# Kernel tuning notes

Hardware: AMD Instinct MI355X
Metric: run time of the kernel (lower is better)

Reference implementation:

```python
import jax, jax.numpy as jnp
import numpy as np

K = 5  # spline kernel size per dim (dim=3 -> 125 kernels)
N1, E1 = 10000, 60000
N2, E2 = 2500, 15000
N3, E3 = 625, 3750
N4, E4 = 160, 960
NC = 4  # num part classes (ShapeNet 'Pistol')


def spline_conv(x, ei, u, W, R, b):
    """SplineConv with degree-1 open B-splines, dim=3, kernel_size=K.
    x: [N, in], ei: [2, E] (src, dst), u: [E, 3] pseudo coords in [0,1],
    W: [K^3, in, out], R: [in, out] root weight, b: [out] bias.
    Mean-normalized neighborhood aggregation (norm=True) + root + bias."""
    src, dst = ei[0], ei[1]
    N, E = x.shape[0], ei.shape[1]
    v = u * (K - 1)
    k0f = jnp.clip(jnp.floor(v), 0.0, K - 2)
    f = v - k0f  # fractional offsets in [0, 1]
    k0 = k0f.astype(jnp.int32)
    # Pre-transform node features by every kernel: z[n, k, o]
    z = jnp.einsum('ni,kio->nko', x, W)
    msg = jnp.zeros((E, W.shape[2]), x.dtype)
    for b0 in (0, 1):
        for b1 in (0, 1):
            for b2 in (0, 1):
                idx = (k0[:, 0] + b0) * K * K + (k0[:, 1] + b1) * K + (k0[:, 2] + b2)
                wgt = ((f[:, 0] if b0 else 1.0 - f[:, 0]) *
                       (f[:, 1] if b1 else 1.0 - f[:, 1]) *
                       (f[:, 2] if b2 else 1.0 - f[:, 2]))
                msg = msg + wgt[:, None] * z[src, idx]
    agg = jax.ops.segment_sum(msg, dst, num_segments=N)
    deg = jax.ops.segment_sum(jnp.ones((E,), x.dtype), dst, num_segments=N)
    return agg / jnp.maximum(deg, 1.0)[:, None] + x @ R + b


def _net(x, u1, u2, u3, u4, w1, r1, b1, w12, r12, b12, w2, r2, b2, w22, r22, b22,
         w3, r3, b3, w32, r32, b32, w4, r4, b4, w42, r42, b42, w5, r5, b5,
         w6, r6, b6, w7, r7, b7, fc1w, fc1b, fc2w, fc2b,
         sk1w, sk1b, sk2w, sk2b, sk3w, sk3b, ei1, ei2, ei3, ei4, c1, c2, c3):
    elu = jax.nn.elu
    h1 = elu(spline_conv(x, ei1, u1, w1, r1, b1))
    h1 = elu(spline_conv(h1, ei1, u1, w12, r12, b12))
    h2 = jnp.concatenate([jax.ops.segment_max(h1, c1, num_segments=N2),
                          jnp.ones((N2, 1), x.dtype)], axis=1)
    h2 = elu(spline_conv(h2, ei2, u2, w2, r2, b2))
    h2 = elu(spline_conv(h2, ei2, u2, w22, r22, b22))
    h3 = jnp.concatenate([jax.ops.segment_max(h2, c2, num_segments=N3),
                          jnp.ones((N3, 1), x.dtype)], axis=1)
    h3 = elu(spline_conv(h3, ei3, u3, w3, r3, b3))
    h3 = elu(spline_conv(h3, ei3, u3, w32, r32, b32))
    h4 = jnp.concatenate([jax.ops.segment_max(h3, c3, num_segments=N4),
                          jnp.ones((N4, 1), x.dtype)], axis=1)
    h4 = elu(spline_conv(h4, ei4, u4, w4, r4, b4))
    h4 = elu(spline_conv(h4, ei4, u4, w42, r42, b42))
    h4 = elu(spline_conv(h4, ei4, u4, w42, r42, b42))  # conv42 applied twice, as in source
    h4 = elu(h4 @ fc1w + fc1b)  # dropout omitted (eval mode)
    g3 = elu(spline_conv(h4[c3] + h3 @ sk3w + sk3b, ei3, u3, w5, r5, b5))
    g2 = elu(spline_conv(g3[c2] + h2 @ sk2w + sk2b, ei2, u2, w6, r6, b6))
    g1 = elu(spline_conv(g2[c1] + h1 @ sk1w + sk1b, ei1, u1, w7, r7, b7))
    return jax.nn.log_softmax(g1 @ fc2w + fc2b, axis=1)


def setup_inputs() -> dict:
    key = jax.random.key(0)
    ks = iter(jax.random.split(key, 96))

    def nrm(shape, s=0.1):
        return jax.random.normal(next(ks), shape, jnp.float32) * s

    def edges(E, N):
        return jax.random.randint(next(ks), (2, E), 0, N, dtype=jnp.int32)

    def clus(Nl, Nn):
        # surjective cluster assignment so every pooled voxel is non-empty
        extra = jax.random.randint(next(ks), (Nl - Nn,), 0, Nn, dtype=jnp.int32)
        return jnp.concatenate([jnp.arange(Nn, dtype=jnp.int32), extra])

    d = {}
    d['x'] = nrm((N1, 1), 1.0)
    d['ei1'], d['u1'] = edges(E1, N1), jax.random.uniform(next(ks), (E1, 3), jnp.float32)
    d['ei2'], d['u2'] = edges(E2, N2), jax.random.uniform(next(ks), (E2, 3), jnp.float32)
    d['ei3'], d['u3'] = edges(E3, N3), jax.random.uniform(next(ks), (E3, 3), jnp.float32)
    d['ei4'], d['u4'] = edges(E4, N4), jax.random.uniform(next(ks), (E4, 3), jnp.float32)
    d['c1'], d['c2'], d['c3'] = clus(N1, N2), clus(N2, N3), clus(N3, N4)
    KK = K ** 3
    for name, cin, cout in [('1', 1, 64), ('12', 64, 64), ('2', 65, 64), ('22', 64, 64),
                            ('3', 65, 64), ('32', 64, 64), ('4', 65, 64), ('42', 64, 64),
                            ('5', 32, 32), ('6', 32, 32), ('7', 32, 32)]:
        d['w' + name] = nrm((KK, cin, cout))
        d['r' + name] = nrm((cin, cout))
        d['b' + name] = jnp.zeros((cout,), jnp.float32)
    d['fc1w'], d['fc1b'] = nrm((64, 32)), jnp.zeros((32,), jnp.float32)
    d['fc2w'], d['fc2b'] = nrm((32, NC)), jnp.zeros((NC,), jnp.float32)
    for s in ('1', '2', '3'):
        d['sk' + s + 'w'] = nrm((64, 32))
        d['sk' + s + 'b'] = jnp.zeros((32,), jnp.float32)
    return d


def reference(x, u1, u2, u3, u4, w1, r1, b1, w12, r12, b12, w2, r2, b2, w22, r22, b22,
              w3, r3, b3, w32, r32, b32, w4, r4, b4, w42, r42, b42, w5, r5, b5,
              w6, r6, b6, w7, r7, b7, fc1w, fc1b, fc2w, fc2b,
              sk1w, sk1b, sk2w, sk2b, sk3w, sk3b, ei1, ei2, ei3, ei4, c1, c2, c3):
    return _net(x, u1, u2, u3, u4, w1, r1, b1, w12, r12, b12, w2, r2, b2, w22, r22, b22,
                w3, r3, b3, w32, r32, b32, w4, r4, b4, w42, r42, b42, w5, r5, b5,
                w6, r6, b6, w7, r7, b7, fc1w, fc1b, fc2w, fc2b,
                sk1w, sk1b, sk2w, sk2b, sk3w, sk3b, ei1, ei2, ei3, ei4, c1, c2, c3)
```

## Files before the change

kernel.cpp:

```cpp
#include <hip/hip_runtime.h>
#include <math.h>


static const int N1 = 10000, E1 = 60000;
static const int N2 = 2500,  E2 = 15000;
static const int N3 = 625,   E3 = 3750;
static const int N4 = 160,   E4 = 960;
static const int NC = 4;
static const int CHUNK = 64;

typedef __attribute__((ext_vector_type(8))) short bfrag;
typedef __attribute__((ext_vector_type(4))) float f32x4;

__device__ __forceinline__ float eluf(float x) { return x > 0.f ? x : expm1f(x); }

__device__ __forceinline__ unsigned short bfc(float f) {
    unsigned u = __float_as_uint(f);
    return (unsigned short)((u + 0x7FFF + ((u >> 16) & 1)) >> 16);
}

struct InitArgs {
    const float* wsrc[10]; unsigned short* wdst[10];
    int cinmat[10], xs_[10], cout[10];
    long welems[10];
    long wtot;
    float* pools[3]; int pM[3];
    float* agg; int aggN4;
    int* preblk; int preN;
    int bB, bC, bD;
};

__global__ __launch_bounds__(256) void init_misc(InitArgs A) {
    const int blk = blockIdx.x, tid = threadIdx.x;
    if (blk < A.bB) {
        const long t = (long)blk * 256 + tid;
        if (t >= A.wtot) return;
        int k = 0;
        while (t >= A.welems[k]) ++k;
        const long base = k ? A.welems[k - 1] : 0;
        const long i2 = t - base;
        const int co = A.cout[k], cm = A.cinmat[k], xs = A.xs_[k];
        const int o = (int)(i2 % co);
        const long rest = i2 / co;
        const int i = (int)(rest % cm);
        const int kk = (int)(rest / cm);
        const float v = A.wsrc[k][((size_t)kk * xs + i) * co + o];
        const int KG = cm >> 3;
        A.wdst[k][(((size_t)(kk * KG + (i >> 3))) * co + o) * 8 + (i & 7)] = bfc(v);
    } else if (blk < A.bC) {
        const int t = (blk - A.bB) * 256 + tid;
        if (t >= A.pM[2]) return;
        const int p = (t < A.pM[0]) ? 0 : (t < A.pM[1] ? 1 : 2);
        const int base = p ? A.pM[p - 1] : 0;
        const int i2 = t - base;
        A.pools[p][i2] = (i2 % 65 == 64) ? 1.0f : -INFINITY;
    } else if (blk < A.bD) {
        const int t = (blk - A.bC) * 256 + tid;
        if (t < A.aggN4) ((float4*)A.agg)[t] = make_float4(0.f, 0.f, 0.f, 0.f);
    } else {
        const int t = (blk - A.bD) * 256 + tid;
        if (t < A.preN) A.preblk[t] = 0;
    }
}

struct Levels {
    const float* u[4]; const int* ei[4]; int E[4];
    int nb0[5];
    int cb0[5];
    int mc[4];
    int* ek0[4]; int* hist[4]; int* cursor[4]; float* deg[4];
    int* bchunk0[4]; int* ck0[4]; int* ccnt[4]; int* perm[4];
};

__global__ __launch_bounds__(256) void prep_conv1(Levels L, const float* __restrict__ x,
                                                  const float* __restrict__ w1,
                                                  float* __restrict__ agg, int nbTot) {
    __shared__ int lh[64];
    const int tid = threadIdx.x;
    if ((int)blockIdx.x < nbTot) {
        int l = 0;
        while (l < 3 && (int)blockIdx.x >= L.nb0[l + 1]) ++l;
        const int bl = blockIdx.x - L.nb0[l];
        if (tid < 64) lh[tid] = 0;
        __syncthreads();
        const int e = bl * 256 + tid;
        if (e < L.E[l]) {
            int b = 0;
            #pragma unroll
            for (int d = 0; d < 3; ++d) {
                const float v = L.u[l][e * 3 + d] * 4.0f;
                const float kf = fminf(fmaxf(floorf(v), 0.f), 3.f);
                b = (b << 2) | (int)kf;
            }
            L.ek0[l][e] = b;
            atomicAdd(&lh[b], 1);
            atomicAdd(&L.deg[l][L.ei[l][L.E[l] + e]], 1.0f);
        }
        __syncthreads();
        if (tid < 64 && lh[tid]) atomicAdd(&L.hist[l][tid], lh[tid]);
    } else {
        const int t = (blockIdx.x - nbTot) * 256 + tid;
        const int e = t >> 6, o = t & 63;
        if (e >= E1) return;
        const int src = L.ei[0][e], dst = L.ei[0][E1 + e];
        float f[3]; int kb = 0;
        #pragma unroll
        for (int d = 0; d < 3; ++d) {
            const float v = L.u[0][e * 3 + d] * 4.0f;
            const float kf = fminf(fmaxf(floorf(v), 0.f), 3.f);
            f[d] = v - kf; kb = kb * 5 + (int)kf;
        }
        float s = 0.f;
        #pragma unroll
        for (int c = 0; c < 8; ++c) {
            const int b0 = (c >> 2) & 1, b1 = (c >> 1) & 1, b2 = c & 1;
            const float wgt = (b0 ? f[0] : 1.f - f[0]) * (b1 ? f[1] : 1.f - f[1]) *
                              (b2 ? f[2] : 1.f - f[2]);
            s += wgt * w1[(size_t)(kb + b0 * 25 + b1 * 5 + b2) * 64 + o];
        }
        atomicAdd(&agg[(size_t)dst * 64 + o], x[src] * s);
    }
}

__global__ void scan_all(Levels L) {
    const int l = blockIdx.x;
    __shared__ int sb[65];
    const int t = threadIdx.x;
    if (t == 0) {
        int cc = 0;
        for (int b = 0; b < 64; ++b) { sb[b] = cc; cc += (L.hist[l][b] + CHUNK - 1) / CHUNK; }
        sb[64] = cc;
    }
    __syncthreads();
    L.bchunk0[l][t] = sb[t];
    if (t == 0) L.bchunk0[l][64] = sb[64];
}

__global__ __launch_bounds__(256) void fill_scatter_node1(
        Levels L, const float* __restrict__ x, float* __restrict__ agg,
        const float* __restrict__ r1, const float* __restrict__ b1,
        float* __restrict__ h1a, int cbTot, int nbTot) {
    __shared__ int lh[64], lbase[64];
    const int tid = threadIdx.x;
    const int blk = blockIdx.x;
    if (blk < cbTot) {
        int l = 0;
        while (l < 3 && blk >= L.cb0[l + 1]) ++l;
        const int c = (blk - L.cb0[l]) * 256 + tid;
        if (c >= L.mc[l]) return;
        const int* bchunk0 = L.bchunk0[l];
        if (c >= bchunk0[64]) { L.ccnt[l][c] = 0; L.ck0[l][c] = 0; return; }
        int lo = 0, hi = 64;
        while (hi - lo > 1) { int m = (lo + hi) >> 1; if (bchunk0[m] <= c) lo = m; else hi = m; }
        const int j = c - bchunk0[lo];
        L.ck0[l][c] = lo;
        L.ccnt[l][c] = min(CHUNK, L.hist[l][lo] - j * CHUNK);
    } else if (blk < cbTot + nbTot) {
        const int fb = blk - cbTot;
        int l = 0;
        while (l < 3 && fb >= L.nb0[l + 1]) ++l;
        const int bl = fb - L.nb0[l];
        if (tid < 64) lh[tid] = 0;
        __syncthreads();
        const int e = bl * 256 + tid;
        int b = -1, r = 0;
        if (e < L.E[l]) { b = L.ek0[l][e]; r = atomicAdd(&lh[b], 1); }
        __syncthreads();
        if (tid < 64) lbase[tid] = lh[tid] ? atomicAdd(&L.cursor[l][tid], lh[tid]) : 0;
        __syncthreads();
        if (e < L.E[l]) L.perm[l][L.bchunk0[l][b] * CHUNK + lbase[b] + r] = e;
    } else {
        const int nb = blk - cbTot - nbTot;
        const int lane = tid & 63;
        const int grp  = tid >> 6;
        const int n = nb * 4 + grp;
        if (n >= N1) return;
        const float d = fmaxf(L.deg[0][n], 1.f);
        const size_t idx = (size_t)n * 64 + lane;
        float s = agg[idx] / d + b1[lane];
        agg[idx] = 0.f;
        s += x[n] * r1[lane];
        h1a[idx] = eluf(s);
    }
}

template<int CINMAT, int COUT, bool HAS_ONES>
__global__ __launch_bounds__(256) void bucket_gemm(
        const float* __restrict__ x, const int* __restrict__ ei, const float* __restrict__ u,
        const unsigned short* __restrict__ Wt, const float* __restrict__ Wf,
        const int* __restrict__ perm, const int* __restrict__ ck0, const int* __restrict__ ccnt,
        float* __restrict__ agg, int E) {
    constexpr int ALDA = CINMAT + 8;
    constexpr int KG   = CINMAT / 8;
    constexpr int NT   = COUT / 16;
    constexpr int HALVES = CINMAT / 32;
    constexpr int XS   = CINMAT + (HAS_ONES ? 1 : 0);
    constexpr int IT   = CINMAT / 4;

    __shared__ unsigned short A0s[64 * ALDA], A1s[64 * ALDA];
    __shared__ float gS[64 * 4], sS[64 * 2];
    __shared__ int srcS[64], dstS[64];
    __shared__ float WonesS[HAS_ONES ? 8 * COUT : 4];

    const int chunk = blockIdx.x;
    const int cnt = ccnt[chunk];
    if (cnt == 0) return;
    const int b = ck0[chunk];
    const int kbase = ((b >> 4) & 3) * 25 + ((b >> 2) & 3) * 5 + (b & 3);
    const int cstart = chunk * CHUNK;
    const int tid = threadIdx.x;

    if (tid < CHUNK) {
        const int e = tid;
        const int pe = (e < cnt) ? perm[cstart + e] : -1;
        int sv = -1, dv = 0;
        float g0 = 0, g1 = 0, g2 = 0, g3 = 0, s0 = 0, s1 = 0;
        if (pe >= 0) {
            sv = ei[pe]; dv = ei[E + pe];
            float f[3];
            #pragma unroll
            for (int d2 = 0; d2 < 3; ++d2) {
                const float v = u[pe * 3 + d2] * 4.f;
                const float kf = fminf(fmaxf(floorf(v), 0.f), 3.f);
                f[d2] = v - kf;
            }
            g0 = (1.f - f[0]) * (1.f - f[1]); g1 = (1.f - f[0]) * f[1];
            g2 = f[0] * (1.f - f[1]);         g3 = f[0] * f[1];
            s0 = 1.f - f[2]; s1 = f[2];
        }
        srcS[e] = sv; dstS[e] = dv;
        gS[e * 4 + 0] = g0; gS[e * 4 + 1] = g1; gS[e * 4 + 2] = g2; gS[e * 4 + 3] = g3;
        sS[e * 2 + 0] = s0; sS[e * 2 + 1] = s1;
    }
    if (HAS_ONES) {
        for (int t2 = tid; t2 < 8 * COUT; t2 += 256) {
            const int c = t2 / COUT, o = t2 % COUT;
            const int koff = ((c >> 2) & 1) * 25 + ((c >> 1) & 1) * 5 + (c & 1);
            WonesS[t2] = Wf[((size_t)(kbase + koff) * XS + CINMAT) * COUT + o];
        }
    }
    __syncthreads();

    {
        const int e  = tid >> 2;
        const int ib = (tid & 3) * IT;
        const int sv = srcS[e];
        const float sc0 = sS[e * 2], sc1 = sS[e * 2 + 1];
        #pragma unroll
        for (int j = 0; j < IT; j += 2) {
            float x0 = 0.f, x1 = 0.f;
            if (sv >= 0) {
                x0 = x[(size_t)sv * XS + ib + j];
                x1 = x[(size_t)sv * XS + ib + j + 1];
            }
            const unsigned p0 = bfc(x0 * sc0) | ((unsigned)bfc(x1 * sc0) << 16);
            const unsigned p1 = bfc(x0 * sc1) | ((unsigned)bfc(x1 * sc1) << 16);
            *(unsigned*)&A0s[e * ALDA + ib + j] = p0;
            *(unsigned*)&A1s[e * ALDA + ib + j] = p1;
        }
    }
    __syncthreads();

    const int lane = tid & 63;
    const int wid  = tid >> 6;
    const int m0   = wid * 16;
    const int arow = m0 + (lane & 15);
    const int kg   = lane >> 4;
    const int ocol = lane & 15;

    f32x4 acc[4][NT];
    #pragma unroll
    for (int q = 0; q < 4; ++q)
        #pragma unroll
        for (int nt = 0; nt < NT; ++nt) acc[q][nt] = (f32x4){0.f, 0.f, 0.f, 0.f};

    #pragma unroll
    for (int q = 0; q < 4; ++q) {
        #pragma unroll
        for (int b2 = 0; b2 < 2; ++b2) {
            const unsigned short* Ab = b2 ? A1s : A0s;
            const int koff = (q >> 1) * 25 + (q & 1) * 5 + b2;
            #pragma unroll
            for (int hf = 0; hf < HALVES; ++hf) {
                const bfrag a = *(const bfrag*)(Ab + arow * ALDA + hf * 32 + kg * 8);
                const int krow = (kbase + koff) * KG + hf * 4 + kg;
                #pragma unroll
                for (int nt = 0; nt < NT; ++nt) {
                    const bfrag bb = *(const bfrag*)(Wt + ((size_t)krow * COUT + nt * 16 + ocol) * 8);
                    acc[q][nt] = __builtin_amdgcn_mfma_f32_16x16x32_bf16(a, bb, acc[q][nt], 0, 0, 0);
                }
            }
        }
    }

    const int grp = lane >> 4;
    #pragma unroll
    for (int nt = 0; nt < NT; ++nt) {
        const int o = nt * 16 + ocol;
        float wo[8];
        if (HAS_ONES) {
            #pragma unroll
            for (int c = 0; c < 8; ++c) wo[c] = WonesS[c * COUT + o];
        }
        #pragma unroll
        for (int r = 0; r < 4; ++r) {
            const int e = m0 + grp * 4 + r;
            if (e < cnt) {
                const float g0 = gS[e * 4 + 0], g1 = gS[e * 4 + 1];
                const float g2 = gS[e * 4 + 2], g3 = gS[e * 4 + 3];
                float v = g0 * acc[0][nt][r] + g1 * acc[1][nt][r] +
                          g2 * acc[2][nt][r] + g3 * acc[3][nt][r];
                if (HAS_ONES) {
                    const float s0v = sS[e * 2], s1v = sS[e * 2 + 1];
                    v += g0 * (s0v * wo[0] + s1v * wo[1]) + g1 * (s0v * wo[2] + s1v * wo[3]) +
                         g2 * (s0v * wo[4] + s1v * wo[5]) + g3 * (s0v * wo[6] + s1v * wo[7]);
                }
                atomicAdd(&agg[(size_t)dstS[e] * COUT + o], v);
            }
        }
    }
}

enum { NODE_PLAIN = 0, NODE_SEGMAX = 1, NODE_FC1 = 2, NODE_LSM = 3 };

template<int CIN, int COUT, int MODE>
__global__ void spline_node_f(const float* __restrict__ x, float* __restrict__ agg,
                              const float* __restrict__ deg, const float* __restrict__ R,
                              const float* __restrict__ b, float* __restrict__ out, int N,
                              const int* __restrict__ cl, float* __restrict__ pool,
                              const float* __restrict__ fw, const float* __restrict__ fb2,
                              float* __restrict__ fout) {
    constexpr int NPB = 256 / COUT;
    __shared__ float rowbuf[NPB][COUT];
    const int lane = threadIdx.x % COUT;
    const int grp  = threadIdx.x / COUT;
    const int n = blockIdx.x * NPB + grp;
    if (n >= N) return;
    const float d = fmaxf(deg[n], 1.f);
    const size_t idx = (size_t)n * COUT + lane;
    float s = agg[idx] / d + b[lane];
    agg[idx] = 0.f;
    const float* xs = x + (size_t)n * CIN;
    #pragma unroll 4
    for (int i = 0; i < CIN; ++i) s += xs[i] * R[i * COUT + lane];
    const float val = eluf(s);
    if (MODE == NODE_PLAIN || MODE == NODE_SEGMAX) out[idx] = val;
    if (MODE == NODE_SEGMAX) {
        float* addr = pool + (size_t)cl[n] * 65 + lane;
        if (val >= 0.f) atomicMax((int*)addr, __float_as_int(val));
        else            atomicMin((unsigned int*)addr, __float_as_uint(val));
    }
    if (MODE == NODE_FC1) {
        rowbuf[grp][lane] = val;
        if (lane < 32) {
            float s2 = fb2[lane];
            #pragma unroll 4
            for (int i = 0; i < 64; ++i) s2 += rowbuf[grp][i] * fw[i * 32 + lane];
            fout[(size_t)n * 32 + lane] = eluf(s2);
        }
    }
    if (MODE == NODE_LSM) {
        float p[NC];
        #pragma unroll
        for (int o = 0; o < NC; ++o) p[o] = val * fw[lane * NC + o];
        #pragma unroll
        for (int m = 16; m >= 1; m >>= 1)
            #pragma unroll
            for (int o = 0; o < NC; ++o) p[o] += __shfl_xor(p[o], m, 32);
        #pragma unroll
        for (int o = 0; o < NC; ++o) p[o] += fb2[o];
        const float mx = fmaxf(fmaxf(p[0], p[1]), fmaxf(p[2], p[3]));
        float se = 0.f;
        #pragma unroll
        for (int o = 0; o < NC; ++o) se += expf(p[o] - mx);
        const float lg = logf(se);
        if (lane < NC) fout[(size_t)n * NC + lane] = p[lane] - mx - lg;
    }
}

__global__ void skip_gather(const float* __restrict__ up, const int* __restrict__ cl,
                            const float* __restrict__ h, const float* __restrict__ skw,
                            const float* __restrict__ skb, float* __restrict__ out, int N) {
    const int lane = threadIdx.x & 31;
    const int grp  = threadIdx.x >> 5;
    const int n = blockIdx.x * 8 + grp;
    if (n >= N) return;
    float s = up[(size_t)cl[n] * 32 + lane] + skb[lane];
    const float* hs = h + (size_t)n * 64;
    #pragma unroll 4
    for (int i = 0; i < 64; ++i) s += hs[i] * skw[i * 32 + lane];
    out[(size_t)n * 32 + lane] = s;
}

struct HLevel {
    const int* ei; const float* u; int E; int maxchunks;
    int *ek0, *hist, *cursor, *bchunk0, *ck0, *ccnt, *perm;
    float* deg;
};

extern "C" void kernel_launch(void* const* d_in, const int* in_sizes, int n_in,
                              void* d_out, int out_size, void* d_ws, size_t ws_size,
                              hipStream_t stream) {
    const float* x    = (const float*)d_in[0];
    const int*   ei1  = (const int*)  d_in[1];
    const float* u1   = (const float*)d_in[2];
    const int*   ei2  = (const int*)  d_in[3];
    const float* u2   = (const float*)d_in[4];
    const int*   ei3  = (const int*)  d_in[5];
    const float* u3   = (const float*)d_in[6];
    const int*   ei4  = (const int*)  d_in[7];
    const float* u4   = (const float*)d_in[8];
    const int*   c1   = (const int*)  d_in[9];
    const int*   c2   = (const int*)  d_in[10];
    const int*   c3   = (const int*)  d_in[11];
    const float *w1  = (const float*)d_in[12], *r1  = (const float*)d_in[13], *b1  = (const float*)d_in[14];
    const float *w12 = (const float*)d_in[15], *r12 = (const float*)d_in[16], *b12 = (const float*)d_in[17];
    const float *w2  = (const float*)d_in[18], *r2  = (const float*)d_in[19], *b2  = (const float*)d_in[20];
    const float *w22 = (const float*)d_in[21], *r22 = (const float*)d_in[22], *b22 = (const float*)d_in[23];
    const float *w3  = (const float*)d_in[24], *r3  = (const float*)d_in[25], *b3  = (const float*)d_in[26];
    const float *w32 = (const float*)d_in[27], *r32 = (const float*)d_in[28], *b32 = (const float*)d_in[29];
    const float *w4  = (const float*)d_in[30], *r4  = (const float*)d_in[31], *b4  = (const float*)d_in[32];
    const float *w42 = (const float*)d_in[33], *r42 = (const float*)d_in[34], *b42 = (const float*)d_in[35];
    const float *w5  = (const float*)d_in[36], *r5  = (const float*)d_in[37], *b5  = (const float*)d_in[38];
    const float *w6  = (const float*)d_in[39], *r6  = (const float*)d_in[40], *b6  = (const float*)d_in[41];
    const float *w7  = (const float*)d_in[42], *r7  = (const float*)d_in[43], *b7  = (const float*)d_in[44];
    const float *fc1w = (const float*)d_in[45], *fc1b = (const float*)d_in[46];
    const float *fc2w = (const float*)d_in[47], *fc2b = (const float*)d_in[48];
    const float *sk1w = (const float*)d_in[49], *sk1b = (const float*)d_in[50];
    const float *sk2w = (const float*)d_in[51], *sk2b = (const float*)d_in[52];
    const float *sk3w = (const float*)d_in[53], *sk3b = (const float*)d_in[54];
    float* out = (float*)d_out;

    char* wsb = (char*)d_ws;
    size_t off = 0;
    auto alloc = [&](size_t bytes) {
        void* p = wsb + off; off = (off + bytes + 255) & ~(size_t)255; return p;
    };
    auto allocF = [&](size_t n) { return (float*)alloc(n * 4); };
    auto allocI = [&](size_t n) { return (int*)alloc(n * 4); };
    auto allocH = [&](size_t n) { return (unsigned short*)alloc(n * 2); };

    float* h1a  = allocF((size_t)N1 * 64);
    float* h1   = allocF((size_t)N1 * 64);
    float* h2in = allocF((size_t)N2 * 65);
    float* h2a  = allocF((size_t)N2 * 64);
    float* h2   = allocF((size_t)N2 * 64);
    float* h3in = allocF((size_t)N3 * 65);
    float* h3a  = allocF((size_t)N3 * 64);
    float* h3   = allocF((size_t)N3 * 64);
    float* h4in = allocF((size_t)N4 * 65);
    float* h4a  = allocF((size_t)N4 * 64);
    float* h4b  = allocF((size_t)N4 * 64);
    float* h4   = allocF((size_t)N4 * 32);
    float* g3in = allocF((size_t)N3 * 32);
    float* g3   = allocF((size_t)N3 * 32);
    float* g2in = allocF((size_t)N2 * 32);
    float* g2   = allocF((size_t)N2 * 32);
    float* g1in = allocF((size_t)N1 * 32);
    float* agg  = allocF((size_t)N1 * 64);

    const size_t SZ64 = (size_t)125 * 8 * 64 * 8;
    const size_t SZ32 = (size_t)125 * 4 * 32 * 8;
    unsigned short* t12 = allocH(SZ64);
    unsigned short* t22 = allocH(SZ64);
    unsigned short* t32 = allocH(SZ64);
    unsigned short* t42 = allocH(SZ64);
    unsigned short* t2  = allocH(SZ64);
    unsigned short* t3  = allocH(SZ64);
    unsigned short* t4  = allocH(SZ64);
    unsigned short* t5  = allocH(SZ32);
    unsigned short* t6  = allocH(SZ32);
    unsigned short* t7  = allocH(SZ32);

    HLevel L[4];
    const int*   eis[4] = {ei1, ei2, ei3, ei4};
    const float* us [4] = {u1, u2, u3, u4};
    const int    Es [4] = {E1, E2, E3, E4};
    const int    Ns [4] = {N1, N2, N3, N4};

    int preN = 0;
    for (int l = 0; l < 4; ++l) preN += 128 + Ns[l];
    int* preblk = allocI(preN);
    {
        int c = 0;
        for (int l = 0; l < 4; ++l) {
            L[l].ei = eis[l]; L[l].u = us[l]; L[l].E = Es[l];
            L[l].maxchunks = (Es[l] + CHUNK - 1) / CHUNK + 64;
            L[l].hist = preblk + c; L[l].cursor = preblk + c + 64;
            L[l].deg = (float*)(preblk + c + 128);
            c += 128 + Ns[l];
            L[l].ek0     = allocI(Es[l]);
            L[l].bchunk0 = allocI(65);
            L[l].ck0     = allocI(L[l].maxchunks);
            L[l].ccnt    = allocI(L[l].maxchunks);
            L[l].perm    = allocI((size_t)L[l].maxchunks * CHUNK);
        }
    }

    InitArgs IA;
    {
        const float* srcs[10] = {w12, w22, w32, w42, w2, w3, w4, w5, w6, w7};
        unsigned short* dsts[10] = {t12, t22, t32, t42, t2, t3, t4, t5, t6, t7};
        const int cms[10] = {64,64,64,64,64,64,64,32,32,32};
        const int xss[10] = {64,64,64,64,65,65,65,32,32,32};
        const int cos[10] = {64,64,64,64,64,64,64,32,32,32};
        long cum = 0;
        for (int k = 0; k < 10; ++k) {
            IA.wsrc[k] = srcs[k]; IA.wdst[k] = dsts[k];
            IA.cinmat[k] = cms[k]; IA.xs_[k] = xss[k]; IA.cout[k] = cos[k];
            cum += (long)125 * cms[k] * cos[k];
            IA.welems[k] = cum;
        }
        IA.wtot = cum;
        IA.pools[0] = h2in; IA.pools[1] = h3in; IA.pools[2] = h4in;
        IA.pM[0] = N2 * 65; IA.pM[1] = N2 * 65 + N3 * 65; IA.pM[2] = N2 * 65 + N3 * 65 + N4 * 65;
        IA.agg = agg; IA.aggN4 = N1 * 64 / 4;
        IA.preblk = preblk; IA.preN = preN;
        const int bA = (int)((IA.wtot + 255) / 256);
        const int bB = (IA.pM[2] + 255) / 256;
        const int bC = (IA.aggN4 + 255) / 256;
        const int bD = (preN + 255) / 256;
        IA.bB = bA; IA.bC = bA + bB; IA.bD = bA + bB + bC;
        init_misc<<<bA + bB + bC + bD, 256, 0, stream>>>(IA);
    }

    Levels DL;
    int nbTot = 0, cbTot = 0;
    {
        for (int l = 0; l < 4; ++l) {
            DL.u[l] = L[l].u; DL.ei[l] = L[l].ei; DL.E[l] = L[l].E;
            DL.nb0[l] = nbTot; nbTot += (L[l].E + 255) / 256;
            DL.cb0[l] = cbTot; cbTot += (L[l].maxchunks + 255) / 256;
            DL.mc[l] = L[l].maxchunks;
            DL.ek0[l] = L[l].ek0; DL.hist[l] = L[l].hist; DL.cursor[l] = L[l].cursor;
            DL.deg[l] = L[l].deg; DL.bchunk0[l] = L[l].bchunk0;
            DL.ck0[l] = L[l].ck0; DL.ccnt[l] = L[l].ccnt; DL.perm[l] = L[l].perm;
        }
        DL.nb0[4] = nbTot; DL.cb0[4] = cbTot;
        const int conv1B = (E1 * 64) / 256;
        prep_conv1<<<nbTot + conv1B, 256, 0, stream>>>(DL, x, w1, agg, nbTot);
        scan_all<<<4, 64, 0, stream>>>(DL);
        const int n1B = (N1 + 3) / 4;
        fill_scatter_node1<<<cbTot + nbTot + n1B, 256, 0, stream>>>(
            DL, x, agg, r1, b1, h1a, cbTot, nbTot);
    }

    bucket_gemm<64, 64, false><<<L[0].maxchunks, 256, 0, stream>>>(
        h1a, L[0].ei, L[0].u, t12, nullptr, L[0].perm, L[0].ck0, L[0].ccnt, agg, L[0].E);
    spline_node_f<64, 64, NODE_SEGMAX><<<(N1 + 3) / 4, 256, 0, stream>>>(
        h1a, agg, L[0].deg, r12, b12, h1, N1, c1, h2in, nullptr, nullptr, nullptr);

    bucket_gemm<64, 64, true><<<L[1].maxchunks, 256, 0, stream>>>(
        h2in, L[1].ei, L[1].u, t2, w2, L[1].perm, L[1].ck0, L[1].ccnt, agg, L[1].E);
    spline_node_f<65, 64, NODE_PLAIN><<<(N2 + 3) / 4, 256, 0, stream>>>(
        h2in, agg, L[1].deg, r2, b2, h2a, N2, nullptr, nullptr, nullptr, nullptr, nullptr);
    bucket_gemm<64, 64, false><<<L[1].maxchunks, 256, 0, stream>>>(
        h2a, L[1].ei, L[1].u, t22, nullptr, L[1].perm, L[1].ck0, L[1].ccnt, agg, L[1].E);
    spline_node_f<64, 64, NODE_SEGMAX><<<(N2 + 3) / 4, 256, 0, stream>>>(
        h2a, agg, L[1].deg, r22, b22, h2, N2, c2, h3in, nullptr, nullptr, nullptr);

    bucket_gemm<64, 64, true><<<L[2].maxchunks, 256, 0, stream>>>(
        h3in, L[2].ei, L[2].u, t3, w3, L[2].perm, L[2].ck0, L[2].ccnt, agg, L[2].E);
    spline_node_f<65, 64, NODE_PLAIN><<<(N3 + 3) / 4, 256, 0, stream>>>(
        h3in, agg, L[2].deg, r3, b3, h3a, N3, nullptr, nullptr, nullptr, nullptr, nullptr);
    bucket_gemm<64, 64, false><<<L[2].maxchunks, 256, 0, stream>>>(
        h3a, L[2].ei, L[2].u, t32, nullptr, L[2].perm, L[2].ck0, L[2].ccnt, agg, L[2].E);
    spline_node_f<64, 64, NODE_SEGMAX><<<(N3 + 3) / 4, 256, 0, stream>>>(
        h3a, agg, L[2].deg, r32, b32, h3, N3, c3, h4in, nullptr, nullptr, nullptr);

    bucket_gemm<64, 64, true><<<L[3].maxchunks, 256, 0, stream>>>(
        h4in, L[3].ei, L[3].u, t4, w4, L[3].perm, L[3].ck0, L[3].ccnt, agg, L[3].E);
    spline_node_f<65, 64, NODE_PLAIN><<<(N4 + 3) / 4, 256, 0, stream>>>(
        h4in, agg, L[3].deg, r4, b4, h4a, N4, nullptr, nullptr, nullptr, nullptr, nullptr);
    bucket_gemm<64, 64, false><<<L[3].maxchunks, 256, 0, stream>>>(
        h4a, L[3].ei, L[3].u, t42, nullptr, L[3].perm, L[3].ck0, L[3].ccnt, agg, L[3].E);
    spline_node_f<64, 64, NODE_PLAIN><<<(N4 + 3) / 4, 256, 0, stream>>>(
        h4a, agg, L[3].deg, r42, b42, h4b, N4, nullptr, nullptr, nullptr, nullptr, nullptr);
    bucket_gemm<64, 64, false><<<L[3].maxchunks, 256, 0, stream>>>(
        h4b, L[3].ei, L[3].u, t42, nullptr, L[3].perm, L[3].ck0, L[3].ccnt, agg, L[3].E);
    spline_node_f<64, 64, NODE_FC1><<<(N4 + 3) / 4, 256, 0, stream>>>(
        h4b, agg, L[3].deg, r42, b42, nullptr, N4, nullptr, nullptr, fc1w, fc1b, h4);

    skip_gather<<<(N3 + 7) / 8, 256, 0, stream>>>(h4, c3, h3, sk3w, sk3b, g3in, N3);
    bucket_gemm<32, 32, false><<<L[2].maxchunks, 256, 0, stream>>>(
        g3in, L[2].ei, L[2].u, t5, nullptr, L[2].perm, L[2].ck0, L[2].ccnt, agg, L[2].E);
    spline_node_f<32, 32, NODE_PLAIN><<<(N3 + 7) / 8, 256, 0, stream>>>(
        g3in, agg, L[2].deg, r5, b5, g3, N3, nullptr, nullptr, nullptr, nullptr, nullptr);

    skip_gather<<<(N2 + 7) / 8, 256, 0, stream>>>(g3, c2, h2, sk2w, sk2b, g2in, N2);
    bucket_gemm<32, 32, false><<<L[1].maxchunks, 256, 0, stream>>>(
        g2in, L[1].ei, L[1].u, t6, nullptr, L[1].perm, L[1].ck0, L[1].ccnt, agg, L[1].E);
    spline_node_f<32, 32, NODE_PLAIN><<<(N2 + 7) / 8, 256, 0, stream>>>(
        g2in, agg, L[1].deg, r6, b6, g2, N2, nullptr, nullptr, nullptr, nullptr, nullptr);

    skip_gather<<<(N1 + 7) / 8, 256, 0, stream>>>(g2, c1, h1, sk1w, sk1b, g1in, N1);
    bucket_gemm<32, 32, false><<<L[0].maxchunks, 256, 0, stream>>>(
        g1in, L[0].ei, L[0].u, t7, nullptr, L[0].perm, L[0].ck0, L[0].ccnt, agg, L[0].E);
    spline_node_f<32, 32, NODE_LSM><<<(N1 + 7) / 8, 256, 0, stream>>>(
        g1in, agg, L[0].deg, r7, b7, nullptr, N1, nullptr, nullptr, fc2w, fc2b, out);
}
```

Before: 284.1 us.

## Fuse level-4 convs into one block, fold scan into scatter, vectorize loads

Replaces the six level-4 conv/node launches with a single 1024-thread kernel that loops over chunks per wave and uses block barriers between stages. It also removes the separate scan_all launch by recomputing the chunk prefix in each block of fill_scatter_node1, packs eight bf16 weights per thread in the weight-conversion init, and uses float4 loads for source features in bucket_gemm. The aim is to cut launch overhead and global traffic on the tiny graph levels. In exchange, level 4 runs on one CU only, and every block of the scatter kernel now repeats the serial 64-entry scan.

```diff
diff --git a/kernel.cpp b/kernel.cpp
--- a/kernel.cpp
+++ b/kernel.cpp
@@ -37,16 +37,18 @@
         if (t >= A.wtot) return;
         int k = 0;
         while (t >= A.welems[k]) ++k;
-        const long base = k ? A.welems[k - 1] : 0;
-        const long i2 = t - base;
+        const long i2 = t - (k ? A.welems[k - 1] : 0);
         const int co = A.cout[k], cm = A.cinmat[k], xs = A.xs_[k];
+        const int KG = cm >> 3;
         const int o = (int)(i2 % co);
         const long rest = i2 / co;
-        const int i = (int)(rest % cm);
-        const int kk = (int)(rest / cm);
-        const float v = A.wsrc[k][((size_t)kk * xs + i) * co + o];
-        const int KG = cm >> 3;
-        A.wdst[k][(((size_t)(kk * KG + (i >> 3))) * co + o) * 8 + (i & 7)] = bfc(v);
+        const int g8 = (int)(rest % KG);
+        const int kk = (int)(rest / KG);
+        const float* sp = A.wsrc[k] + ((size_t)kk * xs + g8 * 8) * co + o;
+        bfrag bv;
+        #pragma unroll
+        for (int j = 0; j < 8; ++j) bv[j] = (short)bfc(sp[(size_t)j * co]);
+        *(bfrag*)(A.wdst[k] + (((size_t)(kk * KG + g8)) * co + o) * 8) = bv;
     } else if (blk < A.bC) {
         const int t = (blk - A.bB) * 256 + tid;
         if (t >= A.pM[2]) return;
@@ -69,7 +71,7 @@
     int cb0[5];
     int mc[4];
     int* ek0[4]; int* hist[4]; int* cursor[4]; float* deg[4];
-    int* bchunk0[4]; int* ck0[4]; int* ccnt[4]; int* perm[4];
+    int* ck0[4]; int* ccnt[4]; int* perm[4];
 };
 
 __global__ __launch_bounds__(256) void prep_conv1(Levels L, const float* __restrict__ x,
@@ -122,44 +124,43 @@
     }
 }
 
-__global__ void scan_all(Levels L) {
-    const int l = blockIdx.x;
-    __shared__ int sb[65];
-    const int t = threadIdx.x;
-    if (t == 0) {
-        int cc = 0;
-        for (int b = 0; b < 64; ++b) { sb[b] = cc; cc += (L.hist[l][b] + CHUNK - 1) / CHUNK; }
-        sb[64] = cc;
-    }
-    __syncthreads();
-    L.bchunk0[l][t] = sb[t];
-    if (t == 0) L.bchunk0[l][64] = sb[64];
-}
-
 __global__ __launch_bounds__(256) void fill_scatter_node1(
         Levels L, const float* __restrict__ x, float* __restrict__ agg,
         const float* __restrict__ r1, const float* __restrict__ b1,
         float* __restrict__ h1a, int cbTot, int nbTot) {
+    __shared__ int sb[65];
     __shared__ int lh[64], lbase[64];
     const int tid = threadIdx.x;
     const int blk = blockIdx.x;
     if (blk < cbTot) {
         int l = 0;
         while (l < 3 && blk >= L.cb0[l + 1]) ++l;
+        if (tid == 0) {
+            int cc = 0;
+            for (int b = 0; b < 64; ++b) { sb[b] = cc; cc += (L.hist[l][b] + CHUNK - 1) / CHUNK; }
+            sb[64] = cc;
+        }
+        __syncthreads();
         const int c = (blk - L.cb0[l]) * 256 + tid;
-        if (c >= L.mc[l]) return;
-        const int* bchunk0 = L.bchunk0[l];
-        if (c >= bchunk0[64]) { L.ccnt[l][c] = 0; L.ck0[l][c] = 0; return; }
-        int lo = 0, hi = 64;
-        while (hi - lo > 1) { int m = (lo + hi) >> 1; if (bchunk0[m] <= c) lo = m; else hi = m; }
-        const int j = c - bchunk0[lo];
-        L.ck0[l][c] = lo;
-        L.ccnt[l][c] = min(CHUNK, L.hist[l][lo] - j * CHUNK);
+        if (c < L.mc[l]) {
+            if (c >= sb[64]) { L.ccnt[l][c] = 0; L.ck0[l][c] = 0; }
+            else {
+                int lo = 0, hi = 64;
+                while (hi - lo > 1) { int m = (lo + hi) >> 1; if (sb[m] <= c) lo = m; else hi = m; }
+                const int j = c - sb[lo];
+                L.ck0[l][c] = lo;
+                L.ccnt[l][c] = min(CHUNK, L.hist[l][lo] - j * CHUNK);
+            }
+        }
     } else if (blk < cbTot + nbTot) {
         const int fb = blk - cbTot;
         int l = 0;
         while (l < 3 && fb >= L.nb0[l + 1]) ++l;
         const int bl = fb - L.nb0[l];
+        if (tid == 0) {
+            int cc = 0;
+            for (int b = 0; b < 64; ++b) { sb[b] = cc; cc += (L.hist[l][b] + CHUNK - 1) / CHUNK; }
+        }
         if (tid < 64) lh[tid] = 0;
         __syncthreads();
         const int e = bl * 256 + tid;
@@ -168,7 +169,7 @@
         __syncthreads();
         if (tid < 64) lbase[tid] = lh[tid] ? atomicAdd(&L.cursor[l][tid], lh[tid]) : 0;
         __syncthreads();
-        if (e < L.E[l]) L.perm[l][L.bchunk0[l][b] * CHUNK + lbase[b] + r] = e;
+        if (e < L.E[l]) L.perm[l][sb[b] * CHUNK + lbase[b] + r] = e;
     } else {
         const int nb = blk - cbTot - nbTot;
         const int lane = tid & 63;
@@ -246,15 +247,22 @@
         const int ib = (tid & 3) * IT;
         const int sv = srcS[e];
         const float sc0 = sS[e * 2], sc1 = sS[e * 2 + 1];
+        float xv[IT];
+        if ((XS & 3) == 0) {
+            #pragma unroll
+            for (int j = 0; j < IT; j += 4) {
+                float4 q = make_float4(0.f, 0.f, 0.f, 0.f);
+                if (sv >= 0) q = *(const float4*)&x[(size_t)sv * XS + ib + j];
+                xv[j] = q.x; xv[j + 1] = q.y; xv[j + 2] = q.z; xv[j + 3] = q.w;
+            }
+        } else {
+            #pragma unroll
+            for (int j = 0; j < IT; ++j) xv[j] = (sv >= 0) ? x[(size_t)sv * XS + ib + j] : 0.f;
+        }
         #pragma unroll
         for (int j = 0; j < IT; j += 2) {
-            float x0 = 0.f, x1 = 0.f;
-            if (sv >= 0) {
-                x0 = x[(size_t)sv * XS + ib + j];
-                x1 = x[(size_t)sv * XS + ib + j + 1];
-            }
-            const unsigned p0 = bfc(x0 * sc0) | ((unsigned)bfc(x1 * sc0) << 16);
-            const unsigned p1 = bfc(x0 * sc1) | ((unsigned)bfc(x1 * sc1) << 16);
+            const unsigned p0 = bfc(xv[j] * sc0) | ((unsigned)bfc(xv[j + 1] * sc0) << 16);
+            const unsigned p1 = bfc(xv[j] * sc1) | ((unsigned)bfc(xv[j + 1] * sc1) << 16);
             *(unsigned*)&A0s[e * ALDA + ib + j] = p0;
             *(unsigned*)&A1s[e * ALDA + ib + j] = p1;
         }
@@ -321,7 +329,7 @@
     }
 }
 
-enum { NODE_PLAIN = 0, NODE_SEGMAX = 1, NODE_FC1 = 2, NODE_LSM = 3 };
+enum { NODE_PLAIN = 0, NODE_SEGMAX = 1, NODE_LSM = 3 };
 
 template<int CIN, int COUT, int MODE>
 __global__ void spline_node_f(const float* __restrict__ x, float* __restrict__ agg,
@@ -331,7 +339,6 @@
                               const float* __restrict__ fw, const float* __restrict__ fb2,
                               float* __restrict__ fout) {
     constexpr int NPB = 256 / COUT;
-    __shared__ float rowbuf[NPB][COUT];
     const int lane = threadIdx.x % COUT;
     const int grp  = threadIdx.x / COUT;
     const int n = blockIdx.x * NPB + grp;
@@ -344,20 +351,11 @@
     #pragma unroll 4
     for (int i = 0; i < CIN; ++i) s += xs[i] * R[i * COUT + lane];
     const float val = eluf(s);
-    if (MODE == NODE_PLAIN || MODE == NODE_SEGMAX) out[idx] = val;
+    if (MODE != NODE_LSM) out[idx] = val;
     if (MODE == NODE_SEGMAX) {
         float* addr = pool + (size_t)cl[n] * 65 + lane;
         if (val >= 0.f) atomicMax((int*)addr, __float_as_int(val));
         else            atomicMin((unsigned int*)addr, __float_as_uint(val));
-    }
-    if (MODE == NODE_FC1) {
-        rowbuf[grp][lane] = val;
-        if (lane < 32) {
-            float s2 = fb2[lane];
-            #pragma unroll 4
-            for (int i = 0; i < 64; ++i) s2 += rowbuf[grp][i] * fw[i * 32 + lane];
-            fout[(size_t)n * 32 + lane] = eluf(s2);
-        }
     }
     if (MODE == NODE_LSM) {
         float p[NC];
@@ -392,9 +390,195 @@
     out[(size_t)n * 32 + lane] = s;
 }
 
+template<bool HAS_ONES>
+__device__ void l4_conv(const float* __restrict__ xin,
+                        const unsigned short* __restrict__ Wt,
+                        const float* __restrict__ Wf,
+                        const int* __restrict__ ei, const float* __restrict__ u,
+                        const int* __restrict__ perm, const int* __restrict__ ck0,
+                        const int* __restrict__ ccnt, int mc, float* __restrict__ agg,
+                        unsigned short (*A0s)[16 * 72], unsigned short (*A1s)[16 * 72],
+                        float (*gS)[64], float (*sS)[32],
+                        int (*srcS)[16], int (*dstS)[16]) {
+    constexpr int ALDA = 72, KG = 8;
+    constexpr int XS = HAS_ONES ? 65 : 64;
+    const int tid = threadIdx.x;
+    const int w = tid >> 6, lane = tid & 63;
+    const int nrounds = (mc + 15) / 16;
+    for (int rr = 0; rr < nrounds; ++rr) {
+        const int chunk = rr * 16 + w;
+        const int cnt = (chunk < mc) ? ccnt[chunk] : 0;
+        int kbase = 0;
+        if (cnt) {
+            const int b = ck0[chunk];
+            kbase = ((b >> 4) & 3) * 25 + ((b >> 2) & 3) * 5 + (b & 3);
+        }
+        if (cnt && lane < 16) {
+            const int e = lane;
+            const int pe = (e < cnt) ? perm[chunk * CHUNK + e] : -1;
+            int sv = -1, dv = 0;
+            float g0 = 0, g1 = 0, g2 = 0, g3 = 0, s0 = 0, s1 = 0;
+            if (pe >= 0) {
+                sv = ei[pe]; dv = ei[E4 + pe];
+                float f[3];
+                #pragma unroll
+                for (int d2 = 0; d2 < 3; ++d2) {
+                    const float v = u[pe * 3 + d2] * 4.f;
+                    const float kf = fminf(fmaxf(floorf(v), 0.f), 3.f);
+                    f[d2] = v - kf;
+                }
+                g0 = (1.f - f[0]) * (1.f - f[1]); g1 = (1.f - f[0]) * f[1];
+                g2 = f[0] * (1.f - f[1]);         g3 = f[0] * f[1];
+                s0 = 1.f - f[2]; s1 = f[2];
+            }
+            srcS[w][e] = sv; dstS[w][e] = dv;
+            gS[w][e * 4 + 0] = g0; gS[w][e * 4 + 1] = g1;
+            gS[w][e * 4 + 2] = g2; gS[w][e * 4 + 3] = g3;
+            sS[w][e * 2 + 0] = s0; sS[w][e * 2 + 1] = s1;
+        }
+        __syncthreads();
+        if (cnt) {
+            const int e  = lane >> 2;
+            const int ib = (lane & 3) * 16;
+            const int sv = srcS[w][e];
+            const float sc0 = sS[w][e * 2], sc1 = sS[w][e * 2 + 1];
+            #pragma unroll
+            for (int j = 0; j < 16; j += 2) {
+                float x0 = 0.f, x1 = 0.f;
+                if (sv >= 0) {
+                    x0 = xin[(size_t)sv * XS + ib + j];
+                    x1 = xin[(size_t)sv * XS + ib + j + 1];
+                }
+                const unsigned p0 = bfc(x0 * sc0) | ((unsigned)bfc(x1 * sc0) << 16);
+                const unsigned p1 = bfc(x0 * sc1) | ((unsigned)bfc(x1 * sc1) << 16);
+                *(unsigned*)&A0s[w][e * ALDA + ib + j] = p0;
+                *(unsigned*)&A1s[w][e * ALDA + ib + j] = p1;
+            }
+        }
+        __syncthreads();
+        if (cnt) {
+            const int arow = lane & 15;
+            const int kg   = lane >> 4;
+            const int ocol = lane & 15;
+            f32x4 acc[4][4];
+            #pragma unroll
+            for (int q = 0; q < 4; ++q)
+                #pragma unroll
+                for (int nt = 0; nt < 4; ++nt) acc[q][nt] = (f32x4){0.f, 0.f, 0.f, 0.f};
+            #pragma unroll
+            for (int q = 0; q < 4; ++q) {
+                #pragma unroll
+                for (int b2 = 0; b2 < 2; ++b2) {
+                    const unsigned short* Ab = b2 ? A1s[w] : A0s[w];
+                    const int koff = (q >> 1) * 25 + (q & 1) * 5 + b2;
+                    #pragma unroll
+                    for (int hf = 0; hf < 2; ++hf) {
+                        const bfrag a = *(const bfrag*)(Ab + arow * ALDA + hf * 32 + kg * 8);
+                        const int krow = (kbase + koff) * KG + hf * 4 + kg;
+                        #pragma unroll
+                        for (int nt = 0; nt < 4; ++nt) {
+                            const bfrag bb = *(const bfrag*)(Wt + ((size_t)krow * 64 + nt * 16 + ocol) * 8);
+                            acc[q][nt] = __builtin_amdgcn_mfma_f32_16x16x32_bf16(a, bb, acc[q][nt], 0, 0, 0);
+                        }
+                    }
+                }
+            }
+            const int grp = lane >> 4;
+            #pragma unroll
+            for (int nt = 0; nt < 4; ++nt) {
+                const int o = nt * 16 + ocol;
+                float wo[8];
+                if (HAS_ONES) {
+                    #pragma unroll
+                    for (int c = 0; c < 8; ++c) {
+                        const int koff = ((c >> 2) & 1) * 25 + ((c >> 1) & 1) * 5 + (c & 1);
+                        wo[c] = Wf[((size_t)(kbase + koff) * 65 + 64) * 64 + o];
+                    }
+                }
+                #pragma unroll
+                for (int r2 = 0; r2 < 4; ++r2) {
+                    const int e = grp * 4 + r2;
+                    if (e < cnt) {
+                        const float g0 = gS[w][e * 4 + 0], g1 = gS[w][e * 4 + 1];
+                        const float g2 = gS[w][e * 4 + 2], g3 = gS[w][e * 4 + 3];
+                        float v = g0 * acc[0][nt][r2] + g1 * acc[1][nt][r2] +
+                                  g2 * acc[2][nt][r2] + g3 * acc[3][nt][r2];
+                        if (HAS_ONES) {
+                            const float s0v = sS[w][e * 2], s1v = sS[w][e * 2 + 1];
+                            v += g0 * (s0v * wo[0] + s1v * wo[1]) + g1 * (s0v * wo[2] + s1v * wo[3]) +
+                                 g2 * (s0v * wo[4] + s1v * wo[5]) + g3 * (s0v * wo[6] + s1v * wo[7]);
+                        }
+                        atomicAdd(&agg[(size_t)dstS[w][e] * 64 + o], v);
+                    }
+                }
+            }
+        }
+        __syncthreads();
+    }
+}
+
+template<int CIN, bool FC1>
+__device__ void l4_node(const float* __restrict__ xin, float* __restrict__ agg,
+                        const float* __restrict__ deg, const float* __restrict__ R,
+                        const float* __restrict__ bb, float* __restrict__ outp,
+                        const float* __restrict__ fw, const float* __restrict__ fb,
+                        float* __restrict__ fout) {
+    const int tid = threadIdx.x, w = tid >> 6, lane = tid & 63;
+    for (int n = w; n < N4; n += 16) {
+        const float d = fmaxf(deg[n], 1.f);
+        const size_t idx = (size_t)n * 64 + lane;
+        float s = agg[idx] / d + bb[lane];
+        agg[idx] = 0.f;
+        const float* xs = xin + (size_t)n * CIN;
+        #pragma unroll 4
+        for (int i = 0; i < CIN; ++i) s += xs[i] * R[i * 64 + lane];
+        const float val = eluf(s);
+        if (!FC1) {
+            outp[idx] = val;
+        } else {
+            float s2 = fb[lane & 31];
+            #pragma unroll 4
+            for (int i = 0; i < 64; ++i) {
+                const float vi = __shfl(val, i, 64);
+                s2 += vi * fw[i * 32 + (lane & 31)];
+            }
+            if (lane < 32) fout[(size_t)n * 32 + lane] = eluf(s2);
+        }
+    }
+}
+
+__global__ __launch_bounds__(1024, 1) void level4_fused(
+        const int* __restrict__ ei, const float* __restrict__ u,
+        const int* __restrict__ perm, const int* __restrict__ ck0,
+        const int* __restrict__ ccnt, int mc,
+        float* __restrict__ agg, const float* __restrict__ deg,
+        const float* __restrict__ h4in,
+        const unsigned short* __restrict__ t4, const float* __restrict__ w4f,
+        const unsigned short* __restrict__ t42,
+        const float* __restrict__ r4, const float* __restrict__ b4,
+        const float* __restrict__ r42, const float* __restrict__ b42,
+        const float* __restrict__ fc1w, const float* __restrict__ fc1b,
+        float* __restrict__ h4a, float* __restrict__ h4b, float* __restrict__ h4) {
+    __shared__ unsigned short A0s[16][16 * 72], A1s[16][16 * 72];
+    __shared__ float gS[16][64], sS[16][32];
+    __shared__ int srcS[16][16], dstS[16][16];
+
+    l4_conv<true >(h4in, t4,  w4f,     ei, u, perm, ck0, ccnt, mc, agg, A0s, A1s, gS, sS, srcS, dstS);
+    __syncthreads();
+    l4_node<65, false>(h4in, agg, deg, r4,  b4,  h4a, nullptr, nullptr, nullptr);
+    __syncthreads();
+    l4_conv<false>(h4a,  t42, nullptr, ei, u, perm, ck0, ccnt, mc, agg, A0s, A1s, gS, sS, srcS, dstS);
+    __syncthreads();
+    l4_node<64, false>(h4a, agg, deg, r42, b42, h4b, nullptr, nullptr, nullptr);
+    __syncthreads();
+    l4_conv<false>(h4b,  t42, nullptr, ei, u, perm, ck0, ccnt, mc, agg, A0s, A1s, gS, sS, srcS, dstS);
+    __syncthreads();
+    l4_node<64, true >(h4b, agg, deg, r42, b42, nullptr, fc1w, fc1b, h4);
+}
+
 struct HLevel {
     const int* ei; const float* u; int E; int maxchunks;
-    int *ek0, *hist, *cursor, *bchunk0, *ck0, *ccnt, *perm;
+    int *ek0, *hist, *cursor, *ck0, *ccnt, *perm;
     float* deg;
 };
 
@@ -490,7 +674,6 @@
             L[l].deg = (float*)(preblk + c + 128);
             c += 128 + Ns[l];
             L[l].ek0     = allocI(Es[l]);
-            L[l].bchunk0 = allocI(65);
             L[l].ck0     = allocI(L[l].maxchunks);
             L[l].ccnt    = allocI(L[l].maxchunks);
             L[l].perm    = allocI((size_t)L[l].maxchunks * CHUNK);
@@ -508,7 +691,7 @@
         for (int k = 0; k < 10; ++k) {
             IA.wsrc[k] = srcs[k]; IA.wdst[k] = dsts[k];
             IA.cinmat[k] = cms[k]; IA.xs_[k] = xss[k]; IA.cout[k] = cos[k];
-            cum += (long)125 * cms[k] * cos[k];
+            cum += (long)125 * (cms[k] / 8) * cos[k];
             IA.welems[k] = cum;
         }
         IA.wtot = cum;
@@ -533,13 +716,12 @@
             DL.cb0[l] = cbTot; cbTot += (L[l].maxchunks + 255) / 256;
             DL.mc[l] = L[l].maxchunks;
             DL.ek0[l] = L[l].ek0; DL.hist[l] = L[l].hist; DL.cursor[l] = L[l].cursor;
-            DL.deg[l] = L[l].deg; DL.bchunk0[l] = L[l].bchunk0;
+            DL.deg[l] = L[l].deg;
             DL.ck0[l] = L[l].ck0; DL.ccnt[l] = L[l].ccnt; DL.perm[l] = L[l].perm;
         }
         DL.nb0[4] = nbTot; DL.cb0[4] = cbTot;
         const int conv1B = (E1 * 64) / 256;
         prep_conv1<<<nbTot + conv1B, 256, 0, stream>>>(DL, x, w1, agg, nbTot);
-        scan_all<<<4, 64, 0, stream>>>(DL);
         const int n1B = (N1 + 3) / 4;
         fill_scatter_node1<<<cbTot + nbTot + n1B, 256, 0, stream>>>(
             DL, x, agg, r1, b1, h1a, cbTot, nbTot);
@@ -568,18 +750,10 @@
     spline_node_f<64, 64, NODE_SEGMAX><<<(N3 + 3) / 4, 256, 0, stream>>>(
         h3a, agg, L[2].deg, r32, b32, h3, N3, c3, h4in, nullptr, nullptr, nullptr);
 
-    bucket_gemm<64, 64, true><<<L[3].maxchunks, 256, 0, stream>>>(
-        h4in, L[3].ei, L[3].u, t4, w4, L[3].perm, L[3].ck0, L[3].ccnt, agg, L[3].E);
-    spline_node_f<65, 64, NODE_PLAIN><<<(N4 + 3) / 4, 256, 0, stream>>>(
-        h4in, agg, L[3].deg, r4, b4, h4a, N4, nullptr, nullptr, nullptr, nullptr, nullptr);
-    bucket_gemm<64, 64, false><<<L[3].maxchunks, 256, 0, stream>>>(
-        h4a, L[3].ei, L[3].u, t42, nullptr, L[3].perm, L[3].ck0, L[3].ccnt, agg, L[3].E);
-    spline_node_f<64, 64, NODE_PLAIN><<<(N4 + 3) / 4, 256, 0, stream>>>(
-        h4a, agg, L[3].deg, r42, b42, h4b, N4, nullptr, nullptr, nullptr, nullptr, nullptr);
-    bucket_gemm<64, 64, false><<<L[3].maxchunks, 256, 0, stream>>>(
-        h4b, L[3].ei, L[3].u, t42, nullptr, L[3].perm, L[3].ck0, L[3].ccnt, agg, L[3].E);
-    spline_node_f<64, 64, NODE_FC1><<<(N4 + 3) / 4, 256, 0, stream>>>(
-        h4b, agg, L[3].deg, r42, b42, nullptr, N4, nullptr, nullptr, fc1w, fc1b, h4);
+    level4_fused<<<1, 1024, 0, stream>>>(
+        L[3].ei, L[3].u, L[3].perm, L[3].ck0, L[3].ccnt, L[3].maxchunks,
+        agg, L[3].deg, h4in, t4, w4, t42, r4, b4, r42, b42, fc1w, fc1b,
+        h4a, h4b, h4);
 
     skip_gather<<<(N3 + 7) / 8, 256, 0, stream>>>(h4, c3, h3, sk3w, sk3b, g3in, N3);
     bucket_gemm<32, 32, false><<<L[2].maxchunks, 256, 0, stream>>>(
```

After: 608.0 us. +114.0%, slower.
